# Optimization experiments

Measured on AMD Instinct MI355X. Metric: run time of the kernel, lower is better.

The kernel has to match this reference:

```python
import jax, jax.numpy as jnp
import numpy as np

N = 50000   # num nodes
E = 800000  # num edges
D = 128     # in_features
C = 1.0     # curvature c
MIN_NORM = 1e-15
BALL_EPS = 4e-3  # float32 boundary eps in PoincareBall.proj


def setup_inputs() -> dict:
    key = jax.random.key(0)
    k1, k2 = jax.random.split(key)
    x = jax.random.normal(k1, (N, D), dtype=jnp.float32)
    edge_index = jax.random.randint(k2, (2, E), 0, N, dtype=jnp.int32)
    return {"x": x, "edge_index": edge_index}


def _expmap0(u, c):
    sqrt_c = c ** 0.5
    u_norm = jnp.maximum(jnp.linalg.norm(u, axis=-1, keepdims=True), MIN_NORM)
    return jnp.tanh(sqrt_c * u_norm) * u / (sqrt_c * u_norm)


def _proj(p, c):
    norm = jnp.maximum(jnp.linalg.norm(p, axis=-1, keepdims=True), MIN_NORM)
    maxnorm = (1.0 - BALL_EPS) / (c ** 0.5)
    return jnp.where(norm > maxnorm, p / norm * maxnorm, p)


def reference(x, edge_index):
    row, col = edge_index[0], edge_index[1]
    # add_remaining_self_loops: drop existing self-loops (weight->0), append N fresh self-loops w=1
    w = jnp.where(row == col, 0.0, 1.0).astype(x.dtype)
    loop = jnp.arange(N, dtype=row.dtype)
    row_f = jnp.concatenate([row, loop])
    col_f = jnp.concatenate([col, loop])
    w_f = jnp.concatenate([w, jnp.ones((N,), x.dtype)])
    # symmetric GCN normalization: D^{-1/2} A D^{-1/2}
    deg = jax.ops.segment_sum(w_f, row_f, num_segments=N)
    dis = jnp.where(deg > 0, 1.0 / jnp.sqrt(jnp.where(deg > 0, deg, 1.0)), 0.0)
    nw = dis[row_f] * w_f * dis[col_f]  # [E+N]
    # gather source features, weighted scatter-add into destination rows
    support = nw[:, None] * x[col_f]                       # [E+N, D]
    result = jax.ops.segment_sum(support, row_f, num_segments=N)  # [N, D]
    return _proj(_expmap0(result, C), C)
```

## Files before the change

### kernel.cpp

```cpp
#include <hip/hip_runtime.h>
#include <math.h>

#define N_NODES 50000
#define N_EDGES 800000
#define DFEAT   128
#define MAXNORM (1.0f - 4e-3f)
#define CAP     32
#define OVF_CAP 8192
#define NPART   8
#define PSIZE   (N_NODES / NPART)
#define SENT    N_NODES

typedef float vfloat4 __attribute__((ext_vector_type(4)));


__device__ __forceinline__ void build_edge(int r, int c, int lo, int hi,
                                           int* __restrict__ deg,
                                           unsigned short* __restrict__ adj16,
                                           int* __restrict__ ovf, int* __restrict__ ovf_cnt) {
    if (r < lo || r >= hi || r == c) return;
    int pos = atomicAdd(&deg[r], 1);
    if (pos < CAP) adj16[r * CAP + pos] = (unsigned short)c;
    else {
        int o = atomicAdd(ovf_cnt, 1);
        if (o < OVF_CAP) { ovf[2 * o] = r; ovf[2 * o + 1] = c; }
    }
}

__global__ void k_build_conv(const int* __restrict__ row, const int* __restrict__ col,
                             const float* __restrict__ x,
                             int* __restrict__ deg, unsigned short* __restrict__ adj16,
                             unsigned int* __restrict__ xb,
                             int* __restrict__ ovf, int* __restrict__ ovf_cnt,
                             int e, int nprep) {
    int gtid = blockIdx.x * blockDim.x + threadIdx.x;
    int nthr = gridDim.x * blockDim.x;
    for (int t = gtid; t < nprep; t += nthr) {
        int node = t >> 4;
        int part = t & 15;
        unsigned int w[4];
        if (node < N_NODES) {
            const vfloat4* x4 = (const vfloat4*)(x + (size_t)node * DFEAT + part * 8);
            vfloat4 a = __builtin_nontemporal_load(x4);
            vfloat4 b = __builtin_nontemporal_load(x4 + 1);
            float fs[8] = {a.x, a.y, a.z, a.w, b.x, b.y, b.z, b.w};
            #pragma unroll
            for (int k = 0; k < 4; ++k) {
                unsigned int lo = __float_as_uint(fs[2 * k]);
                unsigned int hi = __float_as_uint(fs[2 * k + 1]);
                lo = (lo + 0x7FFFu + ((lo >> 16) & 1u)) >> 16;
                hi = (hi + 0x7FFFu + ((hi >> 16) & 1u)) >> 16;
                w[k] = lo | (hi << 16);
            }
        } else {
            w[0] = w[1] = w[2] = w[3] = 0u;
        }
        ((uint4*)xb)[t] = make_uint4(w[0], w[1], w[2], w[3]);
    }

    int p      = blockIdx.x & (NPART - 1);
    int vblock = blockIdx.x >> 3;
    int tpp    = (gridDim.x >> 3) * blockDim.x;
    int tid    = vblock * blockDim.x + threadIdx.x;
    int lo = p * PSIZE, hi = lo + PSIZE;

    int e4 = e >> 2;
    const int4* __restrict__ row4 = (const int4*)row;
    const int4* __restrict__ col4 = (const int4*)col;
    for (int i = tid; i < e4; i += tpp) {
        int4 r4 = row4[i];
        int4 c4 = col4[i];
        build_edge(r4.x, c4.x, lo, hi, deg, adj16, ovf, ovf_cnt);
        build_edge(r4.y, c4.y, lo, hi, deg, adj16, ovf, ovf_cnt);
        build_edge(r4.z, c4.z, lo, hi, deg, adj16, ovf, ovf_cnt);
        build_edge(r4.w, c4.w, lo, hi, deg, adj16, ovf, ovf_cnt);
    }
    for (int i = (e4 << 2) + tid; i < e; i += tpp)
        build_edge(row[i], col[i], lo, hi, deg, adj16, ovf, ovf_cnt);
}

__device__ __forceinline__ float bf_lo(unsigned int w) { return __uint_as_float(w << 16); }
__device__ __forceinline__ float bf_hi(unsigned int w) { return __uint_as_float(w & 0xFFFF0000u); }

__global__ __launch_bounds__(256) void k_gather_bf(const unsigned int* __restrict__ xb,
                                                   const unsigned short* __restrict__ adj16,
                                                   const int* __restrict__ deg,
                                                   const int* __restrict__ ovf,
                                                   const int* __restrict__ ovf_cnt,
                                                   float* __restrict__ out, int n) {
    int lane = threadIdx.x & 63;
    int half = lane >> 5;
    int fl   = lane & 31;
    int rowi = blockIdx.x * 4 + (threadIdx.x >> 6);
    if (rowi >= n) return;

    int cnt    = deg[rowi];
    int capcnt = cnt < CAP ? cnt : CAP;

    int a = SENT;
    if (lane < capcnt) a = (int)adj16[rowi * CAP + lane];

    const unsigned int* __restrict__ xw = xb + 2 * fl;

    uint2 sv = *(const uint2*)(xw + rowi * (DFEAT / 2));

    float acc0 = 0.f, acc1 = 0.f, acc2 = 0.f, acc3 = 0.f;

    {
        int c[8];
        #pragma unroll
        for (int j = 0; j < 8; ++j) c[j] = __shfl(a, 2 * j + half);
        uint2 v[8];
        int   d[8];
        #pragma unroll
        for (int j = 0; j < 8; ++j) { v[j] = *(const uint2*)(xw + c[j] * (DFEAT / 2)); d[j] = deg[c[j]]; }
        #pragma unroll
        for (int j = 0; j < 8; ++j) {
            float wgt = rsqrtf((float)(d[j] + 1));
            acc0 += wgt * bf_lo(v[j].x); acc1 += wgt * bf_hi(v[j].x);
            acc2 += wgt * bf_lo(v[j].y); acc3 += wgt * bf_hi(v[j].y);
        }
    }
    if (capcnt > 16) {
        int c[8];
        #pragma unroll
        for (int j = 0; j < 8; ++j) c[j] = __shfl(a, 16 + 2 * j + half);
        uint2 v[8];
        int   d[8];
        #pragma unroll
        for (int j = 0; j < 8; ++j) { v[j] = *(const uint2*)(xw + c[j] * (DFEAT / 2)); d[j] = deg[c[j]]; }
        #pragma unroll
        for (int j = 0; j < 8; ++j) {
            float wgt = rsqrtf((float)(d[j] + 1));
            acc0 += wgt * bf_lo(v[j].x); acc1 += wgt * bf_hi(v[j].x);
            acc2 += wgt * bf_lo(v[j].y); acc3 += wgt * bf_hi(v[j].y);
        }
    }

    if (cnt > CAP && half == 0) {
        int novf = *ovf_cnt;
        for (int k = 0; k < novf; ++k) {
            if (ovf[2 * k] == rowi) {
                int cc = ovf[2 * k + 1];
                uint2 v = *(const uint2*)(xw + cc * (DFEAT / 2));
                float wgt = rsqrtf((float)(deg[cc] + 1));
                acc0 += wgt * bf_lo(v.x); acc1 += wgt * bf_hi(v.x);
                acc2 += wgt * bf_lo(v.y); acc3 += wgt * bf_hi(v.y);
            }
        }
    }

    acc0 += __shfl_xor(acc0, 32);
    acc1 += __shfl_xor(acc1, 32);
    acc2 += __shfl_xor(acc2, 32);
    acc3 += __shfl_xor(acc3, 32);

    float di = rsqrtf((float)(cnt + 1));

    acc0 += di * bf_lo(sv.x); acc1 += di * bf_hi(sv.x);
    acc2 += di * bf_lo(sv.y); acc3 += di * bf_hi(sv.y);

    acc0 *= di; acc1 *= di; acc2 *= di; acc3 *= di;

    float nsq = acc0 * acc0 + acc1 * acc1 + acc2 * acc2 + acc3 * acc3;
    #pragma unroll
    for (int off = 16; off > 0; off >>= 1) nsq += __shfl_xor(nsq, off);

    float un = fmaxf(sqrtf(nsq), 1e-15f);
    float th = tanhf(un);
    float scale = th / un;
    if (th > MAXNORM) scale *= MAXNORM / th;

    if (half == 0) {
        vfloat4 o = { acc0 * scale, acc1 * scale, acc2 * scale, acc3 * scale };
        __builtin_nontemporal_store(o, (vfloat4*)(out + (size_t)rowi * DFEAT + 4 * fl));
    }
}


#define SCAN_BLK 256
#define NUM_SCAN_BLOCKS ((N_NODES + SCAN_BLK - 1) / SCAN_BLK)

__global__ void k_init_deg(int* __restrict__ deg, int n) {
    int i = blockIdx.x * blockDim.x + threadIdx.x;
    if (i < n) deg[i] = 1;
}

__global__ void k_hist(const int* __restrict__ row, const int* __restrict__ col,
                       int* __restrict__ deg, int e) {
    int i = blockIdx.x * blockDim.x + threadIdx.x;
    if (i < e) {
        int r = row[i], c = col[i];
        if (r != c) atomicAdd(&deg[r], 1);
    }
}

__global__ __launch_bounds__(SCAN_BLK) void k_block_sums(const int* __restrict__ deg,
                                                         int* __restrict__ blockSums, int n) {
    __shared__ int s[SCAN_BLK];
    int t = threadIdx.x;
    int i = blockIdx.x * SCAN_BLK + t;
    s[t] = (i < n) ? (deg[i] - 1) : 0;
    __syncthreads();
    for (int off = SCAN_BLK / 2; off > 0; off >>= 1) {
        if (t < off) s[t] += s[t + off];
        __syncthreads();
    }
    if (t == 0) blockSums[blockIdx.x] = s[0];
}

__global__ __launch_bounds__(SCAN_BLK) void k_scan_blocks(const int* __restrict__ blockSums,
                                                          int* __restrict__ blockBase) {
    __shared__ int s[SCAN_BLK];
    int t = threadIdx.x;
    s[t] = (t < NUM_SCAN_BLOCKS) ? blockSums[t] : 0;
    __syncthreads();
    for (int off = 1; off < SCAN_BLK; off <<= 1) {
        int v = (t >= off) ? s[t - off] : 0;
        __syncthreads();
        s[t] += v;
        __syncthreads();
    }
    if (t < NUM_SCAN_BLOCKS) blockBase[t] = (t == 0) ? 0 : s[t - 1];
}

__global__ __launch_bounds__(SCAN_BLK) void k_block_scan(const int* __restrict__ deg,
                                                         const int* __restrict__ blockBase,
                                                         int* __restrict__ offs,
                                                         int* __restrict__ cursor, int n) {
    __shared__ int s[SCAN_BLK];
    int t = threadIdx.x;
    int i = blockIdx.x * SCAN_BLK + t;
    int cnt = (i < n) ? (deg[i] - 1) : 0;
    s[t] = cnt;
    __syncthreads();
    for (int off = 1; off < SCAN_BLK; off <<= 1) {
        int v = (t >= off) ? s[t - off] : 0;
        __syncthreads();
        s[t] += v;
        __syncthreads();
    }
    if (i < n) {
        int excl = s[t] - cnt + blockBase[blockIdx.x];
        offs[i]   = excl;
        cursor[i] = excl;
    }
}

__global__ void k_scatter(const int* __restrict__ row, const int* __restrict__ col,
                          int* __restrict__ cursor, int* __restrict__ adj, int e) {
    int i = blockIdx.x * blockDim.x + threadIdx.x;
    if (i < e) {
        int r = row[i], c = col[i];
        if (r != c) {
            int pos = atomicAdd(&cursor[r], 1);
            adj[pos] = c;
        }
    }
}

__global__ __launch_bounds__(256) void k_gather_csr(const float* __restrict__ x,
                                                    const int* __restrict__ adj,
                                                    const int* __restrict__ offs,
                                                    const int* __restrict__ deg,
                                                    float* __restrict__ out, int n) {
    int lane = threadIdx.x & 63;
    int rowi = blockIdx.x * 4 + (threadIdx.x >> 6);
    if (rowi >= n) return;

    const float2* __restrict__ x2 = (const float2*)x;
    int beg = offs[rowi];
    int cnt = deg[rowi] - 1;

    float2 acc = make_float2(0.0f, 0.0f);
    for (int base = 0; base < cnt; base += 64) {
        int m = cnt - base; if (m > 64) m = 64;
        int a = 0;
        if (lane < m) a = adj[beg + base + lane];
        for (int nb = 0; nb < m; ++nb) {
            int c = __shfl(a, nb);
            float w = rsqrtf((float)deg[c]);
            float2 v = x2[c * (DFEAT / 2) + lane];
            acc.x += w * v.x;
            acc.y += w * v.y;
        }
    }
    float di = rsqrtf((float)deg[rowi]);
    float2 self = x2[rowi * (DFEAT / 2) + lane];
    acc.x = di * (acc.x + di * self.x);
    acc.y = di * (acc.y + di * self.y);

    float nsq = acc.x * acc.x + acc.y * acc.y;
    #pragma unroll
    for (int off = 32; off > 0; off >>= 1) nsq += __shfl_xor(nsq, off);

    float un = fmaxf(sqrtf(nsq), 1e-15f);
    float th = tanhf(un);
    float scale = th / un;
    if (th > MAXNORM) scale *= MAXNORM / th;

    float2 o = make_float2(acc.x * scale, acc.y * scale);
    ((float2*)out)[rowi * (DFEAT / 2) + lane] = o;
}


extern "C" void kernel_launch(void* const* d_in, const int* in_sizes, int n_in,
                              void* d_out, int out_size, void* d_ws, size_t ws_size,
                              hipStream_t stream) {
    const float* x          = (const float*)d_in[0];
    const int*   edge_index = (const int*)d_in[1];
    const int*   row = edge_index;
    const int*   col = edge_index + N_EDGES;
    float* out = (float*)d_out;
    char*  ws  = (char*)d_ws;

    size_t sz_xb    = sizeof(unsigned short) * (size_t)(N_NODES + 1) * DFEAT;
    size_t sz_adj16 = sizeof(unsigned short) * (size_t)N_NODES * CAP;
    size_t sz_deg   = sizeof(int) * (size_t)N_NODES;
    size_t need = sz_xb + sz_adj16 + sz_deg + sizeof(int) * (1 + 2 * (size_t)OVF_CAP);

    dim3 blk(256);
    if (ws_size >= need) {
        size_t off = 0;
        unsigned int*   xb      = (unsigned int*)(ws + off);   off += sz_xb;
        unsigned short* adj16   = (unsigned short*)(ws + off); off += sz_adj16;
        int*            deg     = (int*)(ws + off);            off += sz_deg;
        int*            ovf_cnt = (int*)(ws + off);            off += sizeof(int);
        int*            ovf     = (int*)(ws + off);

        int nprep = (N_NODES + 1) * (DFEAT / 8);
        hipMemsetAsync(deg, 0, sz_deg + sizeof(int), stream);
        k_build_conv<<<dim3(8192), blk, 0, stream>>>(row, col, x, deg, adj16, xb, ovf, ovf_cnt, N_EDGES, nprep);
        k_gather_bf<<<dim3((N_NODES + 3) / 4), blk, 0, stream>>>(xb, adj16, deg, ovf, ovf_cnt, out, N_NODES);
    } else {
        size_t off = 0;
        int* deg       = (int*)(ws + off); off += sizeof(int) * (size_t)N_NODES;
        int* offs      = (int*)(ws + off); off += sizeof(int) * (size_t)N_NODES;
        int* cursor    = (int*)(ws + off); off += sizeof(int) * (size_t)N_NODES;
        int* blockSums = (int*)(ws + off); off += sizeof(int) * (size_t)NUM_SCAN_BLOCKS;
        int* blockBase = (int*)(ws + off); off += sizeof(int) * (size_t)NUM_SCAN_BLOCKS;
        int* adj       = (int*)(ws + off);

        k_init_deg<<<dim3((N_NODES + 255) / 256), blk, 0, stream>>>(deg, N_NODES);
        k_hist<<<dim3((N_EDGES + 255) / 256), blk, 0, stream>>>(row, col, deg, N_EDGES);
        k_block_sums<<<dim3(NUM_SCAN_BLOCKS), dim3(SCAN_BLK), 0, stream>>>(deg, blockSums, N_NODES);
        k_scan_blocks<<<dim3(1), dim3(SCAN_BLK), 0, stream>>>(blockSums, blockBase);
        k_block_scan<<<dim3(NUM_SCAN_BLOCKS), dim3(SCAN_BLK), 0, stream>>>(deg, blockBase, offs, cursor, N_NODES);
        k_scatter<<<dim3((N_EDGES + 255) / 256), blk, 0, stream>>>(row, col, cursor, adj, N_EDGES);
        k_gather_csr<<<dim3((N_NODES + 3) / 4), blk, 0, stream>>>(x, adj, offs, deg, out, N_NODES);
    }
}
```

Before: 150.9 us.

## Fuse memset, build and gather into one cooperative persistent kernel

Replaces the memset plus two kernel launches with a single cooperative kernel of 1024 blocks. Grid-wide syncs separate the phases: zero the degrees, convert features to bf16, build the adjacency, then gather and apply expmap/proj. The goal is to remove launch overhead and inter-kernel gaps. The costs are grid.sync overhead, fewer blocks in flight for the edge build and gather (grid-stride loops instead of 8192 and 12500 blocks), and a cap of 4 blocks per CU from the launch bounds.

Result: slower. 416.6 us (+176.1%).

```diff
diff --git a/kernel.cpp b/kernel.cpp
--- a/kernel.cpp
+++ b/kernel.cpp
@@ -1,5 +1,8 @@
 #include <hip/hip_runtime.h>
+#include <hip/hip_cooperative_groups.h>
 #include <math.h>
+
+namespace cg = cooperative_groups;
 
 #define N_NODES 50000
 #define N_EDGES 800000
@@ -10,14 +13,17 @@
 #define NPART   8
 #define PSIZE   (N_NODES / NPART)
 #define SENT    N_NODES
+#define NPREP   ((N_NODES + 1) * (DFEAT / 8))
+#define COOP_BLOCKS 1024
 
 typedef float vfloat4 __attribute__((ext_vector_type(4)));
 
+__device__ __forceinline__ float bf_lo(unsigned int w) { return __uint_as_float(w << 16); }
+__device__ __forceinline__ float bf_hi(unsigned int w) { return __uint_as_float(w & 0xFFFF0000u); }
 
 __device__ __forceinline__ void build_edge(int r, int c, int lo, int hi,
-                                           int* __restrict__ deg,
-                                           unsigned short* __restrict__ adj16,
-                                           int* __restrict__ ovf, int* __restrict__ ovf_cnt) {
+                                           int* deg, unsigned short* adj16,
+                                           int* ovf, int* ovf_cnt) {
     if (r < lo || r >= hi || r == c) return;
     int pos = atomicAdd(&deg[r], 1);
     if (pos < CAP) adj16[r * CAP + pos] = (unsigned short)c;
@@ -27,15 +33,21 @@
     }
 }
 
-__global__ void k_build_conv(const int* __restrict__ row, const int* __restrict__ col,
-                             const float* __restrict__ x,
-                             int* __restrict__ deg, unsigned short* __restrict__ adj16,
-                             unsigned int* __restrict__ xb,
-                             int* __restrict__ ovf, int* __restrict__ ovf_cnt,
-                             int e, int nprep) {
+__global__ __launch_bounds__(256, 4) void k_fused(const int* __restrict__ row,
+                                                  const int* __restrict__ col,
+                                                  const float* __restrict__ x,
+                                                  int* deg, unsigned short* adj16,
+                                                  unsigned int* __restrict__ xb,
+                                                  int* ovf, int* ovf_cnt,
+                                                  float* __restrict__ out) {
+    cg::grid_group grid = cg::this_grid();
     int gtid = blockIdx.x * blockDim.x + threadIdx.x;
     int nthr = gridDim.x * blockDim.x;
-    for (int t = gtid; t < nprep; t += nthr) {
+
+    for (int i = gtid; i < N_NODES; i += nthr) deg[i] = 0;
+    if (gtid == 0) *ovf_cnt = 0;
+
+    for (int t = gtid; t < NPREP; t += nthr) {
         int node = t >> 4;
         int part = t & 15;
         unsigned int w[4];
@@ -58,122 +70,119 @@
         ((uint4*)xb)[t] = make_uint4(w[0], w[1], w[2], w[3]);
     }
 
-    int p      = blockIdx.x & (NPART - 1);
-    int vblock = blockIdx.x >> 3;
-    int tpp    = (gridDim.x >> 3) * blockDim.x;
-    int tid    = vblock * blockDim.x + threadIdx.x;
-    int lo = p * PSIZE, hi = lo + PSIZE;
-
-    int e4 = e >> 2;
-    const int4* __restrict__ row4 = (const int4*)row;
-    const int4* __restrict__ col4 = (const int4*)col;
-    for (int i = tid; i < e4; i += tpp) {
-        int4 r4 = row4[i];
-        int4 c4 = col4[i];
-        build_edge(r4.x, c4.x, lo, hi, deg, adj16, ovf, ovf_cnt);
-        build_edge(r4.y, c4.y, lo, hi, deg, adj16, ovf, ovf_cnt);
-        build_edge(r4.z, c4.z, lo, hi, deg, adj16, ovf, ovf_cnt);
-        build_edge(r4.w, c4.w, lo, hi, deg, adj16, ovf, ovf_cnt);
-    }
-    for (int i = (e4 << 2) + tid; i < e; i += tpp)
-        build_edge(row[i], col[i], lo, hi, deg, adj16, ovf, ovf_cnt);
-}
-
-__device__ __forceinline__ float bf_lo(unsigned int w) { return __uint_as_float(w << 16); }
-__device__ __forceinline__ float bf_hi(unsigned int w) { return __uint_as_float(w & 0xFFFF0000u); }
-
-__global__ __launch_bounds__(256) void k_gather_bf(const unsigned int* __restrict__ xb,
-                                                   const unsigned short* __restrict__ adj16,
-                                                   const int* __restrict__ deg,
-                                                   const int* __restrict__ ovf,
-                                                   const int* __restrict__ ovf_cnt,
-                                                   float* __restrict__ out, int n) {
+    grid.sync();
+
+    {
+        int p      = blockIdx.x & (NPART - 1);
+        int vblock = blockIdx.x >> 3;
+        int tpp    = (gridDim.x >> 3) * blockDim.x;
+        int tid    = vblock * blockDim.x + threadIdx.x;
+        int lo = p * PSIZE, hi = lo + PSIZE;
+
+        int e4 = N_EDGES >> 2;
+        const int4* row4 = (const int4*)row;
+        const int4* col4 = (const int4*)col;
+        for (int i = tid; i < e4; i += tpp) {
+            int4 r4 = row4[i];
+            int4 c4 = col4[i];
+            build_edge(r4.x, c4.x, lo, hi, deg, adj16, ovf, ovf_cnt);
+            build_edge(r4.y, c4.y, lo, hi, deg, adj16, ovf, ovf_cnt);
+            build_edge(r4.z, c4.z, lo, hi, deg, adj16, ovf, ovf_cnt);
+            build_edge(r4.w, c4.w, lo, hi, deg, adj16, ovf, ovf_cnt);
+        }
+        for (int i = (e4 << 2) + tid; i < N_EDGES; i += tpp)
+            build_edge(row[i], col[i], lo, hi, deg, adj16, ovf, ovf_cnt);
+    }
+
+    grid.sync();
+
     int lane = threadIdx.x & 63;
     int half = lane >> 5;
     int fl   = lane & 31;
-    int rowi = blockIdx.x * 4 + (threadIdx.x >> 6);
-    if (rowi >= n) return;
-
-    int cnt    = deg[rowi];
-    int capcnt = cnt < CAP ? cnt : CAP;
-
-    int a = SENT;
-    if (lane < capcnt) a = (int)adj16[rowi * CAP + lane];
-
-    const unsigned int* __restrict__ xw = xb + 2 * fl;
-
-    uint2 sv = *(const uint2*)(xw + rowi * (DFEAT / 2));
-
-    float acc0 = 0.f, acc1 = 0.f, acc2 = 0.f, acc3 = 0.f;
-
-    {
-        int c[8];
+    int wv   = threadIdx.x >> 6;
+    const unsigned int* xw = xb + 2 * fl;
+
+    for (int rg = blockIdx.x; rg * 4 < N_NODES; rg += gridDim.x) {
+        int rowi = rg * 4 + wv;
+        if (rowi >= N_NODES) continue;
+
+        int cnt    = deg[rowi];
+        int capcnt = cnt < CAP ? cnt : CAP;
+
+        int a = SENT;
+        if (lane < capcnt) a = (int)adj16[rowi * CAP + lane];
+
+        uint2 sv = *(const uint2*)(xw + rowi * (DFEAT / 2));
+
+        float acc0 = 0.f, acc1 = 0.f, acc2 = 0.f, acc3 = 0.f;
+
+        {
+            int c[8];
+            #pragma unroll
+            for (int j = 0; j < 8; ++j) c[j] = __shfl(a, 2 * j + half);
+            uint2 v[8]; int d[8];
+            #pragma unroll
+            for (int j = 0; j < 8; ++j) { v[j] = *(const uint2*)(xw + c[j] * (DFEAT / 2)); d[j] = deg[c[j]]; }
+            #pragma unroll
+            for (int j = 0; j < 8; ++j) {
+                float wgt = rsqrtf((float)(d[j] + 1));
+                acc0 += wgt * bf_lo(v[j].x); acc1 += wgt * bf_hi(v[j].x);
+                acc2 += wgt * bf_lo(v[j].y); acc3 += wgt * bf_hi(v[j].y);
+            }
+        }
+        if (capcnt > 16) {
+            int c[8];
+            #pragma unroll
+            for (int j = 0; j < 8; ++j) c[j] = __shfl(a, 16 + 2 * j + half);
+            uint2 v[8]; int d[8];
+            #pragma unroll
+            for (int j = 0; j < 8; ++j) { v[j] = *(const uint2*)(xw + c[j] * (DFEAT / 2)); d[j] = deg[c[j]]; }
+            #pragma unroll
+            for (int j = 0; j < 8; ++j) {
+                float wgt = rsqrtf((float)(d[j] + 1));
+                acc0 += wgt * bf_lo(v[j].x); acc1 += wgt * bf_hi(v[j].x);
+                acc2 += wgt * bf_lo(v[j].y); acc3 += wgt * bf_hi(v[j].y);
+            }
+        }
+
+        if (cnt > CAP && half == 0) {
+            int novf = *ovf_cnt;
+            for (int k = 0; k < novf; ++k) {
+                if (ovf[2 * k] == rowi) {
+                    int cc = ovf[2 * k + 1];
+                    uint2 v = *(const uint2*)(xw + cc * (DFEAT / 2));
+                    float wgt = rsqrtf((float)(deg[cc] + 1));
+                    acc0 += wgt * bf_lo(v.x); acc1 += wgt * bf_hi(v.x);
+                    acc2 += wgt * bf_lo(v.y); acc3 += wgt * bf_hi(v.y);
+                }
+            }
+        }
+
+        acc0 += __shfl_xor(acc0, 32);
+        acc1 += __shfl_xor(acc1, 32);
+        acc2 += __shfl_xor(acc2, 32);
+        acc3 += __shfl_xor(acc3, 32);
+
+        float di = rsqrtf((float)(cnt + 1));
+
+        acc0 += di * bf_lo(sv.x); acc1 += di * bf_hi(sv.x);
+        acc2 += di * bf_lo(sv.y); acc3 += di * bf_hi(sv.y);
+
+        acc0 *= di; acc1 *= di; acc2 *= di; acc3 *= di;
+
+        float nsq = acc0 * acc0 + acc1 * acc1 + acc2 * acc2 + acc3 * acc3;
         #pragma unroll
-        for (int j = 0; j < 8; ++j) c[j] = __shfl(a, 2 * j + half);
-        uint2 v[8];
-        int   d[8];
-        #pragma unroll
-        for (int j = 0; j < 8; ++j) { v[j] = *(const uint2*)(xw + c[j] * (DFEAT / 2)); d[j] = deg[c[j]]; }
-        #pragma unroll
-        for (int j = 0; j < 8; ++j) {
-            float wgt = rsqrtf((float)(d[j] + 1));
-            acc0 += wgt * bf_lo(v[j].x); acc1 += wgt * bf_hi(v[j].x);
-            acc2 += wgt * bf_lo(v[j].y); acc3 += wgt * bf_hi(v[j].y);
-        }
-    }
-    if (capcnt > 16) {
-        int c[8];
-        #pragma unroll
-        for (int j = 0; j < 8; ++j) c[j] = __shfl(a, 16 + 2 * j + half);
-        uint2 v[8];
-        int   d[8];
-        #pragma unroll
-        for (int j = 0; j < 8; ++j) { v[j] = *(const uint2*)(xw + c[j] * (DFEAT / 2)); d[j] = deg[c[j]]; }
-        #pragma unroll
-        for (int j = 0; j < 8; ++j) {
-            float wgt = rsqrtf((float)(d[j] + 1));
-            acc0 += wgt * bf_lo(v[j].x); acc1 += wgt * bf_hi(v[j].x);
-            acc2 += wgt * bf_lo(v[j].y); acc3 += wgt * bf_hi(v[j].y);
-        }
-    }
-
-    if (cnt > CAP && half == 0) {
-        int novf = *ovf_cnt;
-        for (int k = 0; k < novf; ++k) {
-            if (ovf[2 * k] == rowi) {
-                int cc = ovf[2 * k + 1];
-                uint2 v = *(const uint2*)(xw + cc * (DFEAT / 2));
-                float wgt = rsqrtf((float)(deg[cc] + 1));
-                acc0 += wgt * bf_lo(v.x); acc1 += wgt * bf_hi(v.x);
-                acc2 += wgt * bf_lo(v.y); acc3 += wgt * bf_hi(v.y);
-            }
-        }
-    }
-
-    acc0 += __shfl_xor(acc0, 32);
-    acc1 += __shfl_xor(acc1, 32);
-    acc2 += __shfl_xor(acc2, 32);
-    acc3 += __shfl_xor(acc3, 32);
-
-    float di = rsqrtf((float)(cnt + 1));
-
-    acc0 += di * bf_lo(sv.x); acc1 += di * bf_hi(sv.x);
-    acc2 += di * bf_lo(sv.y); acc3 += di * bf_hi(sv.y);
-
-    acc0 *= di; acc1 *= di; acc2 *= di; acc3 *= di;
-
-    float nsq = acc0 * acc0 + acc1 * acc1 + acc2 * acc2 + acc3 * acc3;
-    #pragma unroll
-    for (int off = 16; off > 0; off >>= 1) nsq += __shfl_xor(nsq, off);
-
-    float un = fmaxf(sqrtf(nsq), 1e-15f);
-    float th = tanhf(un);
-    float scale = th / un;
-    if (th > MAXNORM) scale *= MAXNORM / th;
-
-    if (half == 0) {
-        vfloat4 o = { acc0 * scale, acc1 * scale, acc2 * scale, acc3 * scale };
-        __builtin_nontemporal_store(o, (vfloat4*)(out + (size_t)rowi * DFEAT + 4 * fl));
+        for (int off = 16; off > 0; off >>= 1) nsq += __shfl_xor(nsq, off);
+
+        float un = fmaxf(sqrtf(nsq), 1e-15f);
+        float th = tanhf(un);
+        float scale = th / un;
+        if (th > MAXNORM) scale *= MAXNORM / th;
+
+        if (half == 0) {
+            vfloat4 o = { acc0 * scale, acc1 * scale, acc2 * scale, acc3 * scale };
+            __builtin_nontemporal_store(o, (vfloat4*)(out + (size_t)rowi * DFEAT + 4 * fl));
+        }
     }
 }
 
@@ -328,10 +337,11 @@
         int*            ovf_cnt = (int*)(ws + off);            off += sizeof(int);
         int*            ovf     = (int*)(ws + off);
 
-        int nprep = (N_NODES + 1) * (DFEAT / 8);
-        hipMemsetAsync(deg, 0, sz_deg + sizeof(int), stream);
-        k_build_conv<<<dim3(8192), blk, 0, stream>>>(row, col, x, deg, adj16, xb, ovf, ovf_cnt, N_EDGES, nprep);
-        k_gather_bf<<<dim3((N_NODES + 3) / 4), blk, 0, stream>>>(xb, adj16, deg, ovf, ovf_cnt, out, N_NODES);
+        void* args[] = { (void*)&row, (void*)&col, (void*)&x, (void*)&deg,
+                         (void*)&adj16, (void*)&xb, (void*)&ovf, (void*)&ovf_cnt,
+                         (void*)&out };
+        hipLaunchCooperativeKernel((const void*)k_fused, dim3(COOP_BLOCKS), blk,
+                                   args, 0, stream);
     } else {
         size_t off = 0;
         int* deg       = (int*)(ws + off); off += sizeof(int) * (size_t)N_NODES;
```
